# Kernel tuning notes

Hardware: AMD Instinct MI355X
Metric: run time of the kernel (lower is better)

The kernel has to match this reference:

```python
import jax, jax.numpy as jnp
import numpy as np

B, T, C = 2, 2048, 1024
NH = 16

def setup_inputs() -> dict:
    key = jax.random.key(0)
    ks = jax.random.split(key, 5)
    s = 0.02
    return {
        "x": jax.random.normal(ks[0], (B, T, C), dtype=jnp.float32),
        "w_attn": jax.random.normal(ks[1], (C, 3 * C), dtype=jnp.float32) * s,
        "b_attn": jax.random.normal(ks[2], (3 * C,), dtype=jnp.float32) * s,
        "w_proj": jax.random.normal(ks[3], (C, C), dtype=jnp.float32) * s,
        "b_proj": jax.random.normal(ks[4], (C,), dtype=jnp.float32) * s,
        "n_heads": NH,
    }

def reference(x, w_attn, b_attn, w_proj, b_proj, n_heads):
    Bx, Tx, Cx = x.shape
    hd = Cx // n_heads
    qkv = x @ w_attn + b_attn                      # [B,T,3C]
    q, k, v = jnp.split(qkv, 3, axis=-1)
    # [B,T,H,hd] -> [B,H,T,hd]
    q = q.reshape(Bx, Tx, n_heads, hd).transpose(0, 2, 1, 3)
    k = k.reshape(Bx, Tx, n_heads, hd).transpose(0, 2, 1, 3)
    v = v.reshape(Bx, Tx, n_heads, hd).transpose(0, 2, 1, 3)
    scale = 1.0 / np.sqrt(hd).astype(np.float32)
    att = jnp.einsum('bhqd,bhkd->bhqk', q, k) * scale   # [B,H,T,T]
    causal = jnp.tril(jnp.ones((Tx, Tx), dtype=bool))
    att = jnp.where(causal[None, None], att, -jnp.inf)
    att = jax.nn.softmax(att, axis=-1)
    y = jnp.einsum('bhqk,bhkd->bhqd', att, v)            # [B,H,T,hd]
    y = y.transpose(0, 2, 1, 3).reshape(Bx, Tx, Cx)
    return y @ w_proj + b_proj
```

## Files before the change

kernel.cpp:

```cpp
#include <hip/hip_runtime.h>

typedef __bf16 bf16x8 __attribute__((ext_vector_type(8)));
typedef __bf16 bf16x4 __attribute__((ext_vector_type(4)));
typedef float  f32x4  __attribute__((ext_vector_type(4)));

#define MFMA_BF16(a, b, c) __builtin_amdgcn_mfma_f32_16x16x32_bf16((a), (b), (c), 0, 0, 0)
#define NEG_INF (-1e30f)
#define SCL 0.18033688f

__device__ __forceinline__ void gld16(const void* g, void* l) {
  __builtin_amdgcn_global_load_lds(
      (const __attribute__((address_space(1))) void*)g,
      (__attribute__((address_space(3))) void*)l, 16, 0, 0);
}

__global__ void cast_f32_bf16(const float* __restrict__ in,
                              __bf16* __restrict__ out, int n) {
  int i = (blockIdx.x * 256 + threadIdx.x) * 8;
  if (i >= n) return;
  float4 a = *(const float4*)&in[i];
  float4 b = *(const float4*)&in[i + 4];
  bf16x8 v;
  v[0] = (__bf16)a.x; v[1] = (__bf16)a.y; v[2] = (__bf16)a.z; v[3] = (__bf16)a.w;
  v[4] = (__bf16)b.x; v[5] = (__bf16)b.y; v[6] = (__bf16)b.z; v[7] = (__bf16)b.w;
  *(bf16x8*)&out[i] = v;
}

__global__ void transpose_f32_bf16(const float* __restrict__ in,
                                   __bf16* __restrict__ out, int R, int C) {
  __shared__ float t[32][33];
  int tx = threadIdx.x & 31, ty = threadIdx.x >> 5;
  int x = blockIdx.x * 32 + tx;
  int y0 = blockIdx.y * 32 + ty;
#pragma unroll
  for (int i = 0; i < 4; ++i)
    t[ty + 8 * i][tx] = in[(size_t)(y0 + 8 * i) * C + x];
  __syncthreads();
  int x2 = blockIdx.y * 32 + tx;
#pragma unroll
  for (int i = 0; i < 4; ++i)
    out[(size_t)(blockIdx.x * 32 + ty + 8 * i) * R + x2] = (__bf16)t[tx][ty + 8 * i];
}

#define BN 128
#define BK 64

template <int BMT, typename TC>
__global__ __launch_bounds__(256) void gemm_bt_bias(
    const __bf16* __restrict__ A, const __bf16* __restrict__ Bt,
    const float* __restrict__ bias, TC* __restrict__ Cmat,
    int M, int N, int K) {
  constexpr int NI = BMT / 32;
  __shared__ __align__(16) __bf16 As[BMT * BK];
  __shared__ __align__(16) __bf16 Bs[BN * BK];
  int tid = threadIdx.x;
  int wave = tid >> 6, lane = tid & 63;
  int l16 = lane & 15, quad = lane >> 4;
  int wm = wave >> 1, wn = wave & 1;
  int m0 = blockIdx.y * BMT, n0 = blockIdx.x * BN;

  f32x4 acc[NI][4];
#pragma unroll
  for (int i = 0; i < NI; ++i)
#pragma unroll
    for (int j = 0; j < 4; ++j) acc[i][j] = (f32x4){0.f, 0.f, 0.f, 0.f};

  int row = tid >> 3;
  int kc = ((tid & 7) ^ ((tid >> 3) & 7)) * 8;
  int xr = (l16 & 7) * 8;

  for (int k0 = 0; k0 < K; k0 += BK) {
#pragma unroll
    for (int i = 0; i < NI; ++i)
      gld16(&A[(size_t)(m0 + row + i * 32) * K + k0 + kc],
            (char*)As + (i * 256 + wave * 64) * 16);
#pragma unroll
    for (int j = 0; j < 4; ++j)
      gld16(&Bt[(size_t)(n0 + row + j * 32) * K + k0 + kc],
            (char*)Bs + (j * 256 + wave * 64) * 16);
    __syncthreads();
#pragma unroll
    for (int ks = 0; ks < 2; ++ks) {
      bf16x8 af[NI], bfr[4];
#pragma unroll
      for (int i = 0; i < NI; ++i)
        af[i] = *(const bf16x8*)&As[(wm * (BMT / 2) + i * 16 + l16) * BK +
                                    ((ks * 32 + quad * 8) ^ xr)];
#pragma unroll
      for (int j = 0; j < 4; ++j)
        bfr[j] = *(const bf16x8*)&Bs[(wn * 64 + j * 16 + l16) * BK +
                                     ((ks * 32 + quad * 8) ^ xr)];
#pragma unroll
      for (int i = 0; i < NI; ++i)
#pragma unroll
        for (int j = 0; j < 4; ++j) acc[i][j] = MFMA_BF16(af[i], bfr[j], acc[i][j]);
    }
    __syncthreads();
  }
#pragma unroll
  for (int i = 0; i < NI; ++i) {
#pragma unroll
    for (int j = 0; j < 4; ++j) {
      int col = n0 + wn * 64 + j * 16 + l16;
      float bv = bias[col];
#pragma unroll
      for (int r = 0; r < 4; ++r) {
        int rw = m0 + wm * (BMT / 2) + i * 16 + quad * 4 + r;
        Cmat[(size_t)rw * N + col] = (TC)(acc[i][j][r] + bv);
      }
    }
  }
}

#define BARX do { asm volatile("" ::: "memory"); __builtin_amdgcn_s_barrier(); \
                  asm volatile("" ::: "memory"); } while (0)
#define WLGKM do { asm volatile("s_waitcnt lgkmcnt(0)" ::: "memory"); \
                   __builtin_amdgcn_sched_barrier(0); } while (0)
#define WVM4 asm volatile("s_waitcnt vmcnt(4)" ::: "memory")
#define STA8(SBUF, SKS, T) do { \
    gld16(srcA1 + (size_t)(T) * 64 + (SKS) * 32, (char*)&As[SBUF][SKS][0] + tid * 16); \
    gld16(srcA2 + (size_t)(T) * 64 + (SKS) * 32, (char*)&As[SBUF][SKS][0] + tid * 16 + 8192); \
  } while (0)
#define STB8(SBUF, SKS, T) do { \
    gld16(srcB1 + (size_t)(T) * 64 + (SKS) * 32, (char*)&Bs[SBUF][SKS][0] + tid * 16); \
    gld16(srcB2 + (size_t)(T) * 64 + (SKS) * 32, (char*)&Bs[SBUF][SKS][0] + tid * 16 + 8192); \
  } while (0)
#define LDA4(CBUF, CKS, MQ) do { \
    const __bf16* p_ = &As[CBUF][CKS][(wm * 128 + (MQ) * 64 + l16) * 32 + xrd]; \
    af[0] = *(const bf16x8*)(p_);        af[1] = *(const bf16x8*)(p_ + 512); \
    af[2] = *(const bf16x8*)(p_ + 1024); af[3] = *(const bf16x8*)(p_ + 1536); \
  } while (0)
#define LDB3(CBUF, CKS) do { \
    const __bf16* p_ = &Bs[CBUF][CKS][(wn * 48 + l16) * 32 + xrd]; \
    bfr[0] = *(const bf16x8*)(p_);       bfr[1] = *(const bf16x8*)(p_ + 512); \
    bfr[2] = *(const bf16x8*)(p_ + 1024); \
  } while (0)
#define MM12(MQ) do { \
    __builtin_amdgcn_s_setprio(1); \
    _Pragma("unroll") for (int mi_ = 0; mi_ < 4; ++mi_) \
    _Pragma("unroll") for (int nj_ = 0; nj_ < 3; ++nj_) \
      acc[(MQ) * 4 + mi_][nj_] = MFMA_BF16(af[mi_], bfr[nj_], acc[(MQ) * 4 + mi_][nj_]); \
    __builtin_amdgcn_s_setprio(0); \
  } while (0)

__global__ __launch_bounds__(512, 2) void gemm_qkv_8ph(
    const __bf16* __restrict__ A, const __bf16* __restrict__ Bt,
    const float* __restrict__ bias, __bf16* __restrict__ qkv,
    __bf16* __restrict__ vt) {
  constexpr int GK = 1024, GN = 3072, NT = 16;
  __shared__ __align__(16) __bf16 As[2][2][256 * 32];
  __shared__ __align__(16) __bf16 Bs[2][2][256 * 32];
  const int tid = threadIdx.x;
  const int wave = tid >> 6, lane = tid & 63;
  const int l16 = lane & 15, quad = lane >> 4;
  const int wm = wave >> 2, wn = wave & 3;
  const int m0 = blockIdx.y * 256, n0 = blockIdx.x * 192;

  const int row0 = tid >> 2;
  const int kc = (((tid & 3) ^ ((row0 >> 1) & 3)) * 8);
  const int xrd = (quad ^ ((l16 >> 1) & 3)) * 8;

  const __bf16* srcA1 = A + (size_t)(m0 + row0) * GK + kc;
  const __bf16* srcA2 = srcA1 + (size_t)128 * GK;
  const __bf16* srcB1 = Bt + (size_t)(n0 + row0) * GK + kc;
  const int br2 = (row0 + 128 < 192) ? row0 + 128 : 191;
  const __bf16* srcB2 = Bt + (size_t)(n0 + br2) * GK + kc;

  f32x4 acc[8][3];
#pragma unroll
  for (int m = 0; m < 8; ++m)
#pragma unroll
    for (int n = 0; n < 3; ++n) acc[m][n] = (f32x4){0.f, 0.f, 0.f, 0.f};

  STA8(0, 0, 0); STB8(0, 0, 0);
  STA8(0, 1, 0); STB8(0, 1, 0);
  STA8(1, 0, 1); STB8(1, 0, 1);
  WVM4;
  BARX;

  bf16x8 af[4], bfr[3];
#pragma unroll 1
  for (int i = 0; i < NT / 2; ++i) {
    const int v = 2 * i + 1;
    const int t2 = (2 * i + 2 < NT) ? 2 * i + 2 : NT - 1;
    const int t3 = (2 * i + 3 < NT) ? 2 * i + 3 : NT - 1;
    LDA4(0, 0, 0); LDB3(0, 0); STA8(1, 1, v);
    BARX; WLGKM; MM12(0); BARX;
    LDA4(0, 0, 1); STB8(1, 1, v);
    BARX; WLGKM; MM12(1); BARX;
    LDA4(0, 1, 0); LDB3(0, 1); STA8(0, 0, t2);
    BARX; WLGKM; MM12(0); BARX;
    LDA4(0, 1, 1); STB8(0, 0, t2);
    BARX; WLGKM; MM12(1); WVM4; BARX;
    LDA4(1, 0, 0); LDB3(1, 0); STA8(0, 1, t2);
    BARX; WLGKM; MM12(0); BARX;
    LDA4(1, 0, 1); STB8(0, 1, t2);
    BARX; WLGKM; MM12(1); BARX;
    LDA4(1, 1, 0); LDB3(1, 1); STA8(1, 0, t3);
    BARX; WLGKM; MM12(0); BARX;
    LDA4(1, 1, 1); STB8(1, 0, t3);
    BARX; WLGKM; MM12(1); WVM4; BARX;
  }

#pragma unroll
  for (int n = 0; n < 3; ++n) {
    const int c0 = n0 + wn * 48 + n * 16;
    const int col = c0 + l16;
    const float bv = bias[col];
    if (c0 < 2048) {
#pragma unroll
      for (int m = 0; m < 8; ++m) {
        const int rw = m0 + wm * 128 + m * 16 + quad * 4;
#pragma unroll
        for (int r = 0; r < 4; ++r)
          qkv[(size_t)(rw + r) * GN + col] = (__bf16)(acc[m][n][r] + bv);
      }
    } else {
      const int h = (col - 2048) >> 6, d = col & 63;
#pragma unroll
      for (int m = 0; m < 8; ++m) {
        const int t0 = m0 + wm * 128 + m * 16 + quad * 4;
        const int b = t0 >> 11, tt = t0 & 2047;
        bf16x4 pb;
#pragma unroll
        for (int r = 0; r < 4; ++r) pb[r] = (__bf16)(acc[m][n][r] + bv);
        *(bf16x4*)&vt[(size_t)((b * 16 + h) * 64 + d) * 2048 + tt] = pb;
      }
    }
  }
}

__global__ __launch_bounds__(256) void attn_causal(
    const __bf16* __restrict__ qkv, const __bf16* __restrict__ vt,
    __bf16* __restrict__ y) {
  __shared__ __align__(16) __bf16 Kb[2][64 * 64];
  __shared__ __align__(16) __bf16 Vb[2][64 * 64];
  __shared__ __align__(16) __bf16 Ps[4][16 * 72];
  const int tid = threadIdx.x;
  const int wave = tid >> 6, lane = tid & 63;
  const int l16 = lane & 15, quad = lane >> 4;
  const int bh = blockIdx.x;
  const int b = bh >> 4, h = bh & 15;
  const int RS = 3072;

  const int row0 = tid >> 3;
  const int kcs = ((tid & 7) ^ ((tid >> 3) & 7)) * 8;
  const int xr = (l16 & 7) * 8;
  const __bf16* kbase = qkv + (size_t)(b * 2048) * RS + 1024 + h * 64 + kcs;
  const __bf16* vbase = vt + (size_t)(bh * 64) * 2048 + kcs;

#pragma unroll 1
  for (int phase = 0; phase < 2; ++phase) {
    const int qt = phase ? (31 - (int)blockIdx.y) : (int)blockIdx.y;

    int qrow = b * 2048 + qt * 64 + wave * 16 + l16;
    const __bf16* qbase = qkv + (size_t)qrow * RS + h * 64;
    bf16x8 qf0 = *(const bf16x8*)(qbase + quad * 8);
    bf16x8 qf1 = *(const bf16x8*)(qbase + 32 + quad * 8);

    float l_i = 0.f;
    f32x4 o[4];
#pragma unroll
    for (int j = 0; j < 4; ++j) o[j] = (f32x4){0.f, 0.f, 0.f, 0.f};

#pragma unroll
    for (int i = 0; i < 2; ++i) {
      gld16(kbase + (size_t)(row0 + 32 * i) * RS,
            (char*)Kb[0] + (i * 256 + tid) * 16);
      gld16(vbase + (size_t)(row0 + 32 * i) * 2048,
            (char*)Vb[0] + (i * 256 + tid) * 16);
    }
    __syncthreads();

    for (int kt = 0; kt <= qt; ++kt) {
      const int cur = kt & 1;
      if (kt < qt) {
#pragma unroll
        for (int i = 0; i < 2; ++i) {
          gld16(kbase + (size_t)((kt + 1) * 64 + row0 + 32 * i) * RS,
                (char*)Kb[cur ^ 1] + (i * 256 + tid) * 16);
          gld16(vbase + (size_t)(row0 + 32 * i) * 2048 + (kt + 1) * 64,
                (char*)Vb[cur ^ 1] + (i * 256 + tid) * 16);
        }
      }

      f32x4 s[4];
#pragma unroll
      for (int j = 0; j < 4; ++j) s[j] = (f32x4){0.f, 0.f, 0.f, 0.f};
#pragma unroll
      for (int j = 0; j < 4; ++j) {
        bf16x8 kf0 = *(const bf16x8*)&Kb[cur][(j * 16 + l16) * 64 + ((quad * 8) ^ xr)];
        bf16x8 kf1 = *(const bf16x8*)&Kb[cur][(j * 16 + l16) * 64 + ((32 + quad * 8) ^ xr)];
        s[j] = MFMA_BF16(kf0, qf0, s[j]);
        s[j] = MFMA_BF16(kf1, qf1, s[j]);
      }

      if (kt == qt) {
        int qg = wave * 16 + l16;
#pragma unroll
        for (int j = 0; j < 4; ++j)
#pragma unroll
          for (int r = 0; r < 4; ++r)
            if (j * 16 + quad * 4 + r > qg) s[j][r] = NEG_INF;
      }

#pragma unroll
      for (int j = 0; j < 4; ++j) {
        bf16x4 pb;
#pragma unroll
        for (int r = 0; r < 4; ++r) {
          float p = __builtin_amdgcn_exp2f(s[j][r] * SCL);
          l_i += p;
          pb[r] = (__bf16)p;
        }
        *(bf16x4*)&Ps[wave][l16 * 72 + j * 16 + quad * 4] = pb;
      }

#pragma unroll
      for (int ks = 0; ks < 2; ++ks) {
        bf16x8 pf = *(const bf16x8*)&Ps[wave][l16 * 72 + ks * 32 + quad * 8];
#pragma unroll
        for (int j = 0; j < 4; ++j) {
          bf16x8 vf = *(const bf16x8*)&Vb[cur][(j * 16 + l16) * 64 +
                                              ((ks * 32 + quad * 8) ^ xr)];
          o[j] = MFMA_BF16(pf, vf, o[j]);
        }
      }
      __syncthreads();
    }

    float lred = l_i;
    lred += __shfl_xor(lred, 16);
    lred += __shfl_xor(lred, 32);
    int orow = b * 2048 + qt * 64 + wave * 16 + quad * 4;
#pragma unroll
    for (int r = 0; r < 4; ++r) {
      float inv = 1.f / __shfl(lred, quad * 4 + r);
#pragma unroll
      for (int j = 0; j < 4; ++j)
        y[(size_t)(orow + r) * 1024 + h * 64 + j * 16 + l16] = (__bf16)(o[j][r] * inv);
    }
  }
}

extern "C" void kernel_launch(void* const* d_in, const int* in_sizes, int n_in,
                              void* d_out, int out_size, void* d_ws, size_t ws_size,
                              hipStream_t stream) {
  (void)in_sizes; (void)n_in; (void)out_size; (void)ws_size;
  const float* x      = (const float*)d_in[0];
  const float* w_attn = (const float*)d_in[1];
  const float* b_attn = (const float*)d_in[2];
  const float* w_proj = (const float*)d_in[3];
  const float* b_proj = (const float*)d_in[4];
  float* out = (float*)d_out;

  __bf16* wt_attn = (__bf16*)d_ws;
  __bf16* wt_proj = wt_attn + (size_t)3072 * 1024;
  __bf16* qkv     = wt_proj + (size_t)1024 * 1024;
  __bf16* ybuf    = qkv + (size_t)4096 * 3072;
  __bf16* vtbuf   = ybuf + (size_t)4096 * 1024;

  cast_f32_bf16<<<4096 * 1024 / 2048, 256, 0, stream>>>(x, ybuf, 4096 * 1024);

  transpose_f32_bf16<<<dim3(3072 / 32, 1024 / 32), 256, 0, stream>>>(w_attn, wt_attn, 1024, 3072);
  transpose_f32_bf16<<<dim3(1024 / 32, 1024 / 32), 256, 0, stream>>>(w_proj, wt_proj, 1024, 1024);

  gemm_qkv_8ph<<<dim3(3072 / 192, 4096 / 256), 512, 0, stream>>>(
      ybuf, wt_attn, b_attn, qkv, vtbuf);

  attn_causal<<<dim3(2 * 16, 16), 256, 0, stream>>>(qkv, vtbuf, ybuf);

  gemm_bt_bias<64, float><<<dim3(1024 / BN, 4096 / 64), 256, 0, stream>>>(
      ybuf, wt_proj, b_proj, out, 4096, 1024, 1024);
}
```

Measured before the change: 176.5 us.

## Load K and V fragments directly from global memory, dropping LDS staging

```diff
diff --git a/kernel.cpp b/kernel.cpp
--- a/kernel.cpp
+++ b/kernel.cpp
@@ -233,8 +233,6 @@
 __global__ __launch_bounds__(256) void attn_causal(
     const __bf16* __restrict__ qkv, const __bf16* __restrict__ vt,
     __bf16* __restrict__ y) {
-  __shared__ __align__(16) __bf16 Kb[2][64 * 64];
-  __shared__ __align__(16) __bf16 Vb[2][64 * 64];
   __shared__ __align__(16) __bf16 Ps[4][16 * 72];
   const int tid = threadIdx.x;
   const int wave = tid >> 6, lane = tid & 63;
@@ -243,11 +241,9 @@
   const int b = bh >> 4, h = bh & 15;
   const int RS = 3072;
 
-  const int row0 = tid >> 3;
-  const int kcs = ((tid & 7) ^ ((tid >> 3) & 7)) * 8;
-  const int xr = (l16 & 7) * 8;
-  const __bf16* kbase = qkv + (size_t)(b * 2048) * RS + 1024 + h * 64 + kcs;
-  const __bf16* vbase = vt + (size_t)(bh * 64) * 2048 + kcs;
+  const __bf16* kbase =
+      qkv + (size_t)(b * 2048 + l16) * RS + 1024 + h * 64 + quad * 8;
+  const __bf16* vbase = vt + (size_t)(bh * 64 + l16) * 2048 + quad * 8;
 
 #pragma unroll 1
   for (int phase = 0; phase < 2; ++phase) {
@@ -263,34 +259,15 @@
 #pragma unroll
     for (int j = 0; j < 4; ++j) o[j] = (f32x4){0.f, 0.f, 0.f, 0.f};
 
-#pragma unroll
-    for (int i = 0; i < 2; ++i) {
-      gld16(kbase + (size_t)(row0 + 32 * i) * RS,
-            (char*)Kb[0] + (i * 256 + tid) * 16);
-      gld16(vbase + (size_t)(row0 + 32 * i) * 2048,
-            (char*)Vb[0] + (i * 256 + tid) * 16);
-    }
-    __syncthreads();
-
     for (int kt = 0; kt <= qt; ++kt) {
-      const int cur = kt & 1;
-      if (kt < qt) {
-#pragma unroll
-        for (int i = 0; i < 2; ++i) {
-          gld16(kbase + (size_t)((kt + 1) * 64 + row0 + 32 * i) * RS,
-                (char*)Kb[cur ^ 1] + (i * 256 + tid) * 16);
-          gld16(vbase + (size_t)(row0 + 32 * i) * 2048 + (kt + 1) * 64,
-                (char*)Vb[cur ^ 1] + (i * 256 + tid) * 16);
-        }
-      }
-
       f32x4 s[4];
 #pragma unroll
       for (int j = 0; j < 4; ++j) s[j] = (f32x4){0.f, 0.f, 0.f, 0.f};
 #pragma unroll
       for (int j = 0; j < 4; ++j) {
-        bf16x8 kf0 = *(const bf16x8*)&Kb[cur][(j * 16 + l16) * 64 + ((quad * 8) ^ xr)];
-        bf16x8 kf1 = *(const bf16x8*)&Kb[cur][(j * 16 + l16) * 64 + ((32 + quad * 8) ^ xr)];
+        const __bf16* kp = kbase + (size_t)(kt * 64 + j * 16) * RS;
+        bf16x8 kf0 = *(const bf16x8*)(kp);
+        bf16x8 kf1 = *(const bf16x8*)(kp + 32);
         s[j] = MFMA_BF16(kf0, qf0, s[j]);
         s[j] = MFMA_BF16(kf1, qf1, s[j]);
       }
@@ -321,12 +298,11 @@
         bf16x8 pf = *(const bf16x8*)&Ps[wave][l16 * 72 + ks * 32 + quad * 8];
 #pragma unroll
         for (int j = 0; j < 4; ++j) {
-          bf16x8 vf = *(const bf16x8*)&Vb[cur][(j * 16 + l16) * 64 +
-                                              ((ks * 32 + quad * 8) ^ xr)];
+          bf16x8 vf = *(const bf16x8*)(vbase + (size_t)(j * 16) * 2048 +
+                                       kt * 64 + ks * 32);
           o[j] = MFMA_BF16(pf, vf, o[j]);
         }
       }
-      __syncthreads();
     }
 
     float lred = l_i;
```

Result: slower. 259.8 us (+47.2%).

## Triple-buffer K/V tiles in causal attention with partial vmcnt waits and setprio

Applied to the files above, without the earlier changes.

```diff
diff --git a/kernel.cpp b/kernel.cpp
--- a/kernel.cpp
+++ b/kernel.cpp
@@ -233,8 +233,8 @@
 __global__ __launch_bounds__(256) void attn_causal(
     const __bf16* __restrict__ qkv, const __bf16* __restrict__ vt,
     __bf16* __restrict__ y) {
-  __shared__ __align__(16) __bf16 Kb[2][64 * 64];
-  __shared__ __align__(16) __bf16 Vb[2][64 * 64];
+  __shared__ __align__(16) __bf16 Kb[3][64 * 64];
+  __shared__ __align__(16) __bf16 Vb[3][64 * 64];
   __shared__ __align__(16) __bf16 Ps[4][16 * 72];
   const int tid = threadIdx.x;
   const int wave = tid >> 6, lane = tid & 63;
@@ -264,29 +264,31 @@
     for (int j = 0; j < 4; ++j) o[j] = (f32x4){0.f, 0.f, 0.f, 0.f};
 
 #pragma unroll
-    for (int i = 0; i < 2; ++i) {
-      gld16(kbase + (size_t)(row0 + 32 * i) * RS,
-            (char*)Kb[0] + (i * 256 + tid) * 16);
-      gld16(vbase + (size_t)(row0 + 32 * i) * 2048,
-            (char*)Vb[0] + (i * 256 + tid) * 16);
-    }
-    __syncthreads();
-
+    for (int t = 0; t < 2; ++t)
+#pragma unroll
+      for (int i = 0; i < 2; ++i) {
+        gld16(kbase + (size_t)(t * 64 + row0 + 32 * i) * RS,
+              (char*)Kb[t] + (i * 256 + tid) * 16);
+        gld16(vbase + (size_t)(row0 + 32 * i) * 2048 + t * 64,
+              (char*)Vb[t] + (i * 256 + tid) * 16);
+      }
+    WVM4;
+    BARX;
+
+    int cur = 0, nxt = 2;
     for (int kt = 0; kt <= qt; ++kt) {
-      const int cur = kt & 1;
-      if (kt < qt) {
-#pragma unroll
-        for (int i = 0; i < 2; ++i) {
-          gld16(kbase + (size_t)((kt + 1) * 64 + row0 + 32 * i) * RS,
-                (char*)Kb[cur ^ 1] + (i * 256 + tid) * 16);
-          gld16(vbase + (size_t)(row0 + 32 * i) * 2048 + (kt + 1) * 64,
-                (char*)Vb[cur ^ 1] + (i * 256 + tid) * 16);
-        }
+#pragma unroll
+      for (int i = 0; i < 2; ++i) {
+        gld16(kbase + (size_t)((kt + 2) * 64 + row0 + 32 * i) * RS,
+              (char*)Kb[nxt] + (i * 256 + tid) * 16);
+        gld16(vbase + (size_t)(row0 + 32 * i) * 2048 + (kt + 2) * 64,
+              (char*)Vb[nxt] + (i * 256 + tid) * 16);
       }
 
       f32x4 s[4];
 #pragma unroll
       for (int j = 0; j < 4; ++j) s[j] = (f32x4){0.f, 0.f, 0.f, 0.f};
+      __builtin_amdgcn_s_setprio(1);
 #pragma unroll
       for (int j = 0; j < 4; ++j) {
         bf16x8 kf0 = *(const bf16x8*)&Kb[cur][(j * 16 + l16) * 64 + ((quad * 8) ^ xr)];
@@ -294,6 +296,7 @@
         s[j] = MFMA_BF16(kf0, qf0, s[j]);
         s[j] = MFMA_BF16(kf1, qf1, s[j]);
       }
+      __builtin_amdgcn_s_setprio(0);
 
       if (kt == qt) {
         int qg = wave * 16 + l16;
@@ -316,6 +319,7 @@
         *(bf16x4*)&Ps[wave][l16 * 72 + j * 16 + quad * 4] = pb;
       }
 
+      __builtin_amdgcn_s_setprio(1);
 #pragma unroll
       for (int ks = 0; ks < 2; ++ks) {
         bf16x8 pf = *(const bf16x8*)&Ps[wave][l16 * 72 + ks * 32 + quad * 8];
@@ -326,7 +330,12 @@
           o[j] = MFMA_BF16(pf, vf, o[j]);
         }
       }
-      __syncthreads();
+      __builtin_amdgcn_s_setprio(0);
+
+      WVM4;
+      BARX;
+      cur = (cur + 1 == 3) ? 0 : cur + 1;
+      nxt = (nxt + 1 == 3) ? 0 : nxt + 1;
     }
 
     float lred = l_i;
```

Measured after the change: 179.6 us. About the same (+1.8%).
